# Kernel tuning notes

Measured on AMD Instinct MI355X. Metric: run time of the kernel, lower is better.

The kernel has to match this reference:

```python
import jax, jax.numpy as jnp
import numpy as np

NORMALIZED_LENGTH = 512  # init kwarg
T_FRAMES = 32768
N_LM = 543  # mediapipe holistic landmark count


def setup_inputs() -> dict:
    key = jax.random.key(0)
    kf, kn, kd, ki = jax.random.split(key, 4)
    frames = jax.random.uniform(kf, (T_FRAMES, N_LM, 3), dtype=jnp.float32)
    nan_mask = jax.random.uniform(kn, (T_FRAMES, N_LM, 3)) < 0.10
    frames = jnp.where(nan_mask, jnp.float32(jnp.nan), frames)
    drop = jax.random.uniform(kd, (T_FRAMES,)) < 0.05
    hand_zone = jnp.arange(N_LM) >= 468
    frames = jnp.where(drop[:, None, None] & hand_zone[None, :, None], jnp.float32(jnp.nan), frames)
    lips_idx = jax.random.randint(ki, (40,), 0, 468, dtype=jnp.int32)
    return {"frames": frames, "lips_idx": lips_idx}


def _nan_mean0(x):
    # tf_nan_mean over axis 0 (keepdims); 0/0 -> NaN in TF is immediately zeroed
    # afterwards, so we emit 0 directly (identical forward values, safe grads).
    finite = ~jnp.isnan(x)
    s = jnp.where(finite, x, jnp.zeros((), x.dtype)).sum(axis=0, keepdims=True)
    c = finite.sum(axis=0, keepdims=True)
    return jnp.where(c == 0, jnp.zeros((), x.dtype), s / jnp.maximum(c, 1).astype(x.dtype))


def reference(frames, lips_idx):
    fr = frames[:, :, :2]                       # drop z coord
    lh = fr[:, 468:489]                         # [T, 21, 2]
    rh = fr[:, 522:543]                         # [T, 21, 2]
    lh = jnp.stack([lh[..., 0], 1.0 - lh[..., 1]], axis=-1)
    rh = jnp.stack([1.0 - rh[..., 0], 1.0 - rh[..., 1]], axis=-1)
    # stack hands, NaN->0, sum over the 2-hand axis
    hand = jnp.nan_to_num(lh) + jnp.nan_to_num(rh)   # [T, 21, 2]
    keep = hand.sum(axis=(1, 2)) != 0.0              # frames with >=1 visible hand
    hand = hand[keep]                                # [S, 21, 2]
    lips = fr[:, lips_idx][keep]                     # [S, 40, 2]
    lips = jnp.where(jnp.isnan(lips), _nan_mean0(lips), lips)
    raw = jnp.concatenate([hand, lips], axis=1)      # [S, 61, 2]
    S = int(raw.shape[0])
    # tf.linspace(0, S-1, L+1) cast to int32 -> segment boundaries (truncation)
    b = np.linspace(0.0, S - 1.0, NORMALIZED_LENGTH + 1).astype(np.int32)
    # frame t belongs to bin i with b[i] <= t < b[i+1]; t >= b[L] maps to L (dropped)
    seg = jnp.asarray(np.searchsorted(b, np.arange(S), side="right") - 1)
    sums = jax.ops.segment_sum(raw, seg, num_segments=NORMALIZED_LENGTH)
    cnt = jax.ops.segment_sum(jnp.ones((S,), raw.dtype), seg, num_segments=NORMALIZED_LENGTH)
    # raw is NaN-free at this point, so nan-mean == plain mean; empty bin -> NaN -> 0
    mean = jnp.where(cnt[:, None, None] == 0, jnp.zeros((), raw.dtype),
                     sums / jnp.maximum(cnt, 1.0)[:, None, None])
    sampled = mean.reshape(NORMALIZED_LENGTH, -1)    # Flatten -> [L, 122]
    rows = sampled.sum(axis=1) != 0.0                # drop all-zero (empty) bins
    return sampled[rows]
```

## Files before the change

kernel.cpp:

```cpp
#include <hip/hip_runtime.h>

#define T_FRAMES 32768
#define ROWF 1629
#define NSEG 512
#define NVAL 122
#define PADI 16

__global__ __launch_bounds__(256) void k1_keep(const float* __restrict__ frames,
                                               int* __restrict__ keep) {
  int lane = threadIdx.x & 63;
  int wid = threadIdx.x >> 6;
  int t = blockIdx.x * 4 + wid;
  const float* f = frames + (size_t)t * ROWF;
  float s = 0.0f;
  if (lane < 42) {
    int j = (lane < 21) ? lane : lane - 21;
    int base = ((lane < 21) ? 468 : 522) + j;
    float x = f[base * 3];
    float y = f[base * 3 + 1];
    float ax = (lane < 21) ? x : 1.0f - x;
    float ay = 1.0f - y;
    ax = (ax == ax) ? ax : 0.0f;
    ay = (ay == ay) ? ay : 0.0f;
    s = ax + ay;
  }
  #pragma unroll
  for (int off = 32; off > 0; off >>= 1) s += __shfl_down(s, off);
  if (lane == 0) keep[t] = (s != 0.0f) ? 1 : 0;
}

__global__ __launch_bounds__(1024) void k2_scan(const int* __restrict__ keep,
                                                int* __restrict__ kept_t,
                                                int* __restrict__ Sp) {
  __shared__ int wsum[16];
  int tid = threadIdx.x;
  const int PER = T_FRAMES / 1024;
  int base = tid * PER;
  int fl[PER];
  int local = 0;
  #pragma unroll
  for (int k = 0; k < PER; ++k) { fl[k] = keep[base + k]; local += fl[k]; }

  int lane = tid & 63, wid = tid >> 6;
  int scan = local;
  #pragma unroll
  for (int off = 1; off < 64; off <<= 1) {
    int n = __shfl_up(scan, off);
    if (lane >= off) scan += n;
  }
  if (lane == 63) wsum[wid] = scan;
  __syncthreads();
  if (tid < 16) {
    int v = wsum[tid];
    #pragma unroll
    for (int off = 1; off < 16; off <<= 1) {
      int n = __shfl_up(v, off);
      if (tid >= off) v += n;
    }
    wsum[tid] = v;
  }
  __syncthreads();
  int excl = ((wid == 0) ? 0 : wsum[wid - 1]) + (scan - local);
  #pragma unroll
  for (int k = 0; k < PER; ++k) {
    if (fl[k]) kept_t[excl++] = base + k;
  }
  if (tid == 1023) Sp[0] = wsum[15];
}

__global__ __launch_bounds__(1024) void k3_seg(
    const float* __restrict__ frames, const int* __restrict__ lips_idx,
    const int* __restrict__ kept_t, const int* __restrict__ Sp,
    float* __restrict__ out, int out_size,
    float* __restrict__ seg_ls, int* __restrict__ seg_lc,
    int* __restrict__ seg_n, float* __restrict__ tot_s,
    int* __restrict__ tot_c) {
  __shared__ int seglist[72];
  __shared__ float h_s[42];
  __shared__ float l_s[80];
  __shared__ int   l_c[80];
  int tid = threadIdx.x, lane = tid & 63, wid = tid >> 6;
  int seg = blockIdx.x;
  int S = Sp[0];
  long long M = (long long)S - 1; if (M < 0) M = 0;
  int lo = (int)(((long long)seg * M) >> 9);
  int hi = (int)(((long long)(seg + 1) * M) >> 9);
  int cnt = hi - lo;
  int loadN = cnt + ((seg == NSEG - 1 && S >= 2) ? 1 : 0);

  if (tid < 42) h_s[tid] = 0.0f;
  if (tid < 80) { l_s[tid] = 0.0f; l_c[tid] = 0; }
  if (tid < loadN) seglist[tid] = kept_t[lo + tid];
  __syncthreads();

  int idx1 = 0, idx2 = 0;
  if (lane >= 42) idx1 = lips_idx[lane - 42];
  if (lane < 18)  idx2 = lips_idx[22 + lane];

  float ahx = 0.0f, ahy = 0.0f;
  float a1x = 0.0f, a1y = 0.0f; int c1x = 0, c1y = 0;
  float a2x = 0.0f, a2y = 0.0f; int c2x = 0, c2y = 0;

  for (int k = wid; k < cnt; k += 16) {
    const float* f = frames + (size_t)seglist[k] * ROWF;
    int o1;
    if (lane < 21)      o1 = (468 + lane) * 3;
    else if (lane < 42) o1 = (522 + (lane - 21)) * 3;
    else                o1 = idx1 * 3;
    float x1 = f[o1], y1 = f[o1 + 1];
    float x2 = 0.0f, y2 = 0.0f;
    if (lane < 18) { int o2 = idx2 * 3; x2 = f[o2]; y2 = f[o2 + 1]; }

    float ax = (lane < 21) ? x1 : 1.0f - x1;
    float ay = 1.0f - y1;
    ax = (ax == ax) ? ax : 0.0f;
    ay = (ay == ay) ? ay : 0.0f;
    float bx = __shfl(ax, lane + 21);
    float by = __shfl(ay, lane + 21);
    if (lane < 21) { ahx += ax + bx; ahy += ay + by; }
    if (lane >= 42) {
      if (x1 == x1) { a1x += x1; c1x++; }
      if (y1 == y1) { a1y += y1; c1y++; }
    }
    if (lane < 18) {
      if (x2 == x2) { a2x += x2; c2x++; }
      if (y2 == y2) { a2y += y2; c2y++; }
    }
  }

  if (lane < 21) { atomicAdd(&h_s[2 * lane], ahx); atomicAdd(&h_s[2 * lane + 1], ahy); }
  if (lane >= 42) {
    int j = lane - 42;
    atomicAdd(&l_s[2 * j], a1x); atomicAdd(&l_s[2 * j + 1], a1y);
    atomicAdd(&l_c[2 * j], c1x); atomicAdd(&l_c[2 * j + 1], c1y);
  }
  if (lane < 18) {
    int j = 22 + lane;
    atomicAdd(&l_s[2 * j], a2x); atomicAdd(&l_s[2 * j + 1], a2y);
    atomicAdd(&l_c[2 * j], c2x); atomicAdd(&l_c[2 * j + 1], c2y);
  }
  __syncthreads();

  if (tid < 42) {
    float v = cnt ? h_s[tid] / (float)cnt : 0.0f;
    int o = seg * NVAL + tid;
    if (o < out_size) out[o] = v;
  }
  if (tid < 80) {
    seg_ls[seg * 80 + tid] = l_s[tid];
    seg_lc[seg * 80 + tid] = l_c[tid];
    atomicAdd(&tot_s[tid * PADI], l_s[tid]);
    atomicAdd(&tot_c[tid * PADI], l_c[tid]);
  }
  if (tid == 0) seg_n[seg] = cnt;

  if (seg == NSEG - 1 && S >= 2 && wid == 0 && lane < 40) {
    const float* f = frames + (size_t)seglist[cnt] * ROWF;
    int idx = lips_idx[lane];
    float x = f[idx * 3], y = f[idx * 3 + 1];
    if (x == x) { atomicAdd(&tot_s[(2 * lane) * PADI], x);
                  atomicAdd(&tot_c[(2 * lane) * PADI], 1); }
    if (y == y) { atomicAdd(&tot_s[(2 * lane + 1) * PADI], y);
                  atomicAdd(&tot_c[(2 * lane + 1) * PADI], 1); }
  }
}

__global__ __launch_bounds__(128) void k4_final(
    const float* __restrict__ seg_ls, const int* __restrict__ seg_lc,
    const int* __restrict__ seg_n, const float* __restrict__ tot_s,
    const int* __restrict__ tot_c, float* __restrict__ out, int out_size) {
  int w = threadIdx.x;
  int seg = blockIdx.x;
  if (w >= 80) return;
  int tc = tot_c[w * PADI];
  float cm = tc ? tot_s[w * PADI] / (float)tc : 0.0f;
  int n = seg_n[seg];
  float v = 0.0f;
  if (n) {
    int c = seg_lc[seg * 80 + w];
    v = (seg_ls[seg * 80 + w] + (float)(n - c) * cm) / (float)n;
  }
  int o = seg * NVAL + 42 + w;
  if (o < out_size) out[o] = v;
}

extern "C" void kernel_launch(void* const* d_in, const int* in_sizes, int n_in,
                              void* d_out, int out_size, void* d_ws, size_t ws_size,
                              hipStream_t stream) {
  const float* frames = (const float*)d_in[0];
  const int* lips_idx = (const int*)d_in[1];
  float* out = (float*)d_out;

  char* ws = (char*)d_ws;
  int* keep      = (int*)(ws);
  int* kept_t    = (int*)(ws + 131072);
  int* Sp        = (int*)(ws + 262144);
  float* tot_s   = (float*)(ws + 262208);
  int* tot_c     = (int*)(ws + 267328);
  float* seg_ls  = (float*)(ws + 272448);
  int* seg_lc    = (int*)(ws + 436288);
  int* seg_n     = (int*)(ws + 600128);

  hipMemsetAsync((void*)tot_s, 0, 10240, stream);

  k1_keep<<<8192, 256, 0, stream>>>(frames, keep);
  k2_scan<<<1, 1024, 0, stream>>>(keep, kept_t, Sp);
  k3_seg<<<NSEG, 1024, 0, stream>>>(frames, lips_idx, kept_t, Sp, out, out_size,
                                    seg_ls, seg_lc, seg_n, tot_s, tot_c);
  k4_final<<<NSEG, 128, 0, stream>>>(seg_ls, seg_lc, seg_n, tot_s, tot_c,
                                     out, out_size);
}
```

Before: 300.7 us.

## Fuse keep+scan and seg+final kernels using last-block-done atomic counters

Merges the keep-flag kernel with the single-block scan, and the segment kernel with the finalize kernel. In each case the last block to finish, detected through an atomic counter with threadfences, runs the following stage. This removes two kernel launches and their launch gaps. The trade-off is that the finalize work now runs serially in a single 1024-thread block, and the keep kernel now uses 1024-thread blocks instead of 256.

```diff
diff --git a/kernel.cpp b/kernel.cpp
--- a/kernel.cpp
+++ b/kernel.cpp
@@ -6,16 +6,15 @@
 #define NVAL 122
 #define PADI 16
 
-__global__ __launch_bounds__(256) void k1_keep(const float* __restrict__ frames,
-                                               int* __restrict__ keep) {
-  int lane = threadIdx.x & 63;
-  int wid = threadIdx.x >> 6;
-  int t = blockIdx.x * 4 + wid;
+__global__ __launch_bounds__(1024) void k1_keep_scan(
+    const float* __restrict__ frames, int* __restrict__ keep,
+    int* __restrict__ kept_t, int* __restrict__ Sp, int* __restrict__ ctl) {
+  int tid = threadIdx.x, lane = tid & 63, wid = tid >> 6;
+  int t = blockIdx.x * 16 + wid;
   const float* f = frames + (size_t)t * ROWF;
   float s = 0.0f;
   if (lane < 42) {
-    int j = (lane < 21) ? lane : lane - 21;
-    int base = ((lane < 21) ? 468 : 522) + j;
+    int base = (lane < 21) ? (468 + lane) : (522 + (lane - 21));
     float x = f[base * 3];
     float y = f[base * 3 + 1];
     float ax = (lane < 21) ? x : 1.0f - x;
@@ -27,21 +26,22 @@
   #pragma unroll
   for (int off = 32; off > 0; off >>= 1) s += __shfl_down(s, off);
   if (lane == 0) keep[t] = (s != 0.0f) ? 1 : 0;
-}
-
-__global__ __launch_bounds__(1024) void k2_scan(const int* __restrict__ keep,
-                                                int* __restrict__ kept_t,
-                                                int* __restrict__ Sp) {
+
+  __shared__ int is_last;
+  __threadfence();
+  __syncthreads();
+  if (tid == 0) is_last = (atomicAdd(&ctl[0], 1) == (int)gridDim.x - 1);
+  __syncthreads();
+  if (!is_last) return;
+  __threadfence();
+
   __shared__ int wsum[16];
-  int tid = threadIdx.x;
   const int PER = T_FRAMES / 1024;
   int base = tid * PER;
   int fl[PER];
   int local = 0;
   #pragma unroll
   for (int k = 0; k < PER; ++k) { fl[k] = keep[base + k]; local += fl[k]; }
-
-  int lane = tid & 63, wid = tid >> 6;
   int scan = local;
   #pragma unroll
   for (int off = 1; off < 64; off <<= 1) {
@@ -74,7 +74,7 @@
     float* __restrict__ out, int out_size,
     float* __restrict__ seg_ls, int* __restrict__ seg_lc,
     int* __restrict__ seg_n, float* __restrict__ tot_s,
-    int* __restrict__ tot_c) {
+    int* __restrict__ tot_c, int* __restrict__ ctl) {
   __shared__ int seglist[72];
   __shared__ float h_s[42];
   __shared__ float l_s[80];
@@ -163,25 +163,28 @@
     if (y == y) { atomicAdd(&tot_s[(2 * lane + 1) * PADI], y);
                   atomicAdd(&tot_c[(2 * lane + 1) * PADI], 1); }
   }
-}
-
-__global__ __launch_bounds__(128) void k4_final(
-    const float* __restrict__ seg_ls, const int* __restrict__ seg_lc,
-    const int* __restrict__ seg_n, const float* __restrict__ tot_s,
-    const int* __restrict__ tot_c, float* __restrict__ out, int out_size) {
-  int w = threadIdx.x;
-  int seg = blockIdx.x;
-  if (w >= 80) return;
-  int tc = tot_c[w * PADI];
-  float cm = tc ? tot_s[w * PADI] / (float)tc : 0.0f;
-  int n = seg_n[seg];
-  float v = 0.0f;
-  if (n) {
-    int c = seg_lc[seg * 80 + w];
-    v = (seg_ls[seg * 80 + w] + (float)(n - c) * cm) / (float)n;
-  }
-  int o = seg * NVAL + 42 + w;
-  if (o < out_size) out[o] = v;
+
+  __shared__ int last2;
+  __threadfence();
+  __syncthreads();
+  if (tid == 0) last2 = (atomicAdd(&ctl[16], 1) == NSEG - 1);
+  __syncthreads();
+  if (!last2) return;
+  __threadfence();
+
+  for (int i = tid; i < NSEG * 80; i += 1024) {
+    int sg = i / 80, w = i - sg * 80;
+    int tc = tot_c[w * PADI];
+    float cm = tc ? tot_s[w * PADI] / (float)tc : 0.0f;
+    int n = seg_n[sg];
+    float v = 0.0f;
+    if (n) {
+      int c = seg_lc[sg * 80 + w];
+      v = (seg_ls[sg * 80 + w] + (float)(n - c) * cm) / (float)n;
+    }
+    int o = sg * NVAL + 42 + w;
+    if (o < out_size) out[o] = v;
+  }
 }
 
 extern "C" void kernel_launch(void* const* d_in, const int* in_sizes, int n_in,
@@ -195,18 +198,16 @@
   int* keep      = (int*)(ws);
   int* kept_t    = (int*)(ws + 131072);
   int* Sp        = (int*)(ws + 262144);
-  float* tot_s   = (float*)(ws + 262208);
-  int* tot_c     = (int*)(ws + 267328);
-  float* seg_ls  = (float*)(ws + 272448);
-  int* seg_lc    = (int*)(ws + 436288);
-  int* seg_n     = (int*)(ws + 600128);
-
-  hipMemsetAsync((void*)tot_s, 0, 10240, stream);
-
-  k1_keep<<<8192, 256, 0, stream>>>(frames, keep);
-  k2_scan<<<1, 1024, 0, stream>>>(keep, kept_t, Sp);
+  int* ctl       = (int*)(ws + 262208);
+  float* tot_s   = (float*)(ws + 262336);
+  int* tot_c     = (int*)(ws + 267456);
+  float* seg_ls  = (float*)(ws + 272576);
+  int* seg_lc    = (int*)(ws + 436416);
+  int* seg_n     = (int*)(ws + 600256);
+
+  hipMemsetAsync((void*)ctl, 0, 10368, stream);
+
+  k1_keep_scan<<<2048, 1024, 0, stream>>>(frames, keep, kept_t, Sp, ctl);
   k3_seg<<<NSEG, 1024, 0, stream>>>(frames, lips_idx, kept_t, Sp, out, out_size,
-                                    seg_ls, seg_lc, seg_n, tot_s, tot_c);
-  k4_final<<<NSEG, 128, 0, stream>>>(seg_ls, seg_lc, seg_n, tot_s, tot_c,
-                                     out, out_size);
+                                    seg_ls, seg_lc, seg_n, tot_s, tot_c, ctl);
 }
```

Result: slower. 1.129 ms (+275.4%).

## Replace atomic reductions with per-wave shared partials and single-block final reduce

Applied to the files above, without the earlier changes.

Shared-memory atomics in the segment kernel are replaced by per-wave partial arrays that are summed after the barrier. The global atomic accumulation of lip totals, and the memset that cleared it, are removed. The final kernel becomes one 1024-thread block that reduces the per-segment partials and adds the last kept frame, then writes all outputs. This removes atomic contention and a memset launch, but the final stage now runs on a single block.

```diff
diff --git a/kernel.cpp b/kernel.cpp
--- a/kernel.cpp
+++ b/kernel.cpp
@@ -4,7 +4,7 @@
 #define ROWF 1629
 #define NSEG 512
 #define NVAL 122
-#define PADI 16
+
 
 __global__ __launch_bounds__(256) void k1_keep(const float* __restrict__ frames,
                                                int* __restrict__ keep) {
@@ -14,8 +14,7 @@
   const float* f = frames + (size_t)t * ROWF;
   float s = 0.0f;
   if (lane < 42) {
-    int j = (lane < 21) ? lane : lane - 21;
-    int base = ((lane < 21) ? 468 : 522) + j;
+    int base = (lane < 21) ? (468 + lane) : (522 + (lane - 21));
     float x = f[base * 3];
     float y = f[base * 3 + 1];
     float ax = (lane < 21) ? x : 1.0f - x;
@@ -73,12 +72,11 @@
     const int* __restrict__ kept_t, const int* __restrict__ Sp,
     float* __restrict__ out, int out_size,
     float* __restrict__ seg_ls, int* __restrict__ seg_lc,
-    int* __restrict__ seg_n, float* __restrict__ tot_s,
-    int* __restrict__ tot_c) {
-  __shared__ int seglist[72];
-  __shared__ float h_s[42];
-  __shared__ float l_s[80];
-  __shared__ int   l_c[80];
+    int* __restrict__ seg_n) {
+  __shared__ int seglist[64];
+  __shared__ float hp[16][42];
+  __shared__ float lp[16][80];
+  __shared__ int   cp[16][80];
   int tid = threadIdx.x, lane = tid & 63, wid = tid >> 6;
   int seg = blockIdx.x;
   int S = Sp[0];
@@ -86,11 +84,8 @@
   int lo = (int)(((long long)seg * M) >> 9);
   int hi = (int)(((long long)(seg + 1) * M) >> 9);
   int cnt = hi - lo;
-  int loadN = cnt + ((seg == NSEG - 1 && S >= 2) ? 1 : 0);
-
-  if (tid < 42) h_s[tid] = 0.0f;
-  if (tid < 80) { l_s[tid] = 0.0f; l_c[tid] = 0; }
-  if (tid < loadN) seglist[tid] = kept_t[lo + tid];
+
+  if (tid < cnt) seglist[tid] = kept_t[lo + tid];
   __syncthreads();
 
   int idx1 = 0, idx2 = 0;
@@ -128,60 +123,82 @@
     }
   }
 
-  if (lane < 21) { atomicAdd(&h_s[2 * lane], ahx); atomicAdd(&h_s[2 * lane + 1], ahy); }
+  if (lane < 21) { hp[wid][2 * lane] = ahx; hp[wid][2 * lane + 1] = ahy; }
   if (lane >= 42) {
     int j = lane - 42;
-    atomicAdd(&l_s[2 * j], a1x); atomicAdd(&l_s[2 * j + 1], a1y);
-    atomicAdd(&l_c[2 * j], c1x); atomicAdd(&l_c[2 * j + 1], c1y);
+    lp[wid][2 * j] = a1x; lp[wid][2 * j + 1] = a1y;
+    cp[wid][2 * j] = c1x; cp[wid][2 * j + 1] = c1y;
   }
   if (lane < 18) {
     int j = 22 + lane;
-    atomicAdd(&l_s[2 * j], a2x); atomicAdd(&l_s[2 * j + 1], a2y);
-    atomicAdd(&l_c[2 * j], c2x); atomicAdd(&l_c[2 * j + 1], c2y);
+    lp[wid][2 * j] = a2x; lp[wid][2 * j + 1] = a2y;
+    cp[wid][2 * j] = c2x; cp[wid][2 * j + 1] = c2y;
   }
   __syncthreads();
 
   if (tid < 42) {
-    float v = cnt ? h_s[tid] / (float)cnt : 0.0f;
+    float s = 0.0f;
+    #pragma unroll
+    for (int w = 0; w < 16; ++w) s += hp[w][tid];
+    float v = cnt ? s / (float)cnt : 0.0f;
     int o = seg * NVAL + tid;
     if (o < out_size) out[o] = v;
   }
   if (tid < 80) {
-    seg_ls[seg * 80 + tid] = l_s[tid];
-    seg_lc[seg * 80 + tid] = l_c[tid];
-    atomicAdd(&tot_s[tid * PADI], l_s[tid]);
-    atomicAdd(&tot_c[tid * PADI], l_c[tid]);
+    float s = 0.0f; int c = 0;
+    #pragma unroll
+    for (int w = 0; w < 16; ++w) { s += lp[w][tid]; c += cp[w][tid]; }
+    seg_ls[seg * 80 + tid] = s;
+    seg_lc[seg * 80 + tid] = c;
   }
   if (tid == 0) seg_n[seg] = cnt;
-
-  if (seg == NSEG - 1 && S >= 2 && wid == 0 && lane < 40) {
-    const float* f = frames + (size_t)seglist[cnt] * ROWF;
-    int idx = lips_idx[lane];
-    float x = f[idx * 3], y = f[idx * 3 + 1];
-    if (x == x) { atomicAdd(&tot_s[(2 * lane) * PADI], x);
-                  atomicAdd(&tot_c[(2 * lane) * PADI], 1); }
-    if (y == y) { atomicAdd(&tot_s[(2 * lane + 1) * PADI], y);
-                  atomicAdd(&tot_c[(2 * lane + 1) * PADI], 1); }
-  }
-}
-
-__global__ __launch_bounds__(128) void k4_final(
+}
+
+__global__ __launch_bounds__(1024) void k4_final(
+    const float* __restrict__ frames, const int* __restrict__ lips_idx,
+    const int* __restrict__ kept_t, const int* __restrict__ Sp,
     const float* __restrict__ seg_ls, const int* __restrict__ seg_lc,
-    const int* __restrict__ seg_n, const float* __restrict__ tot_s,
-    const int* __restrict__ tot_c, float* __restrict__ out, int out_size) {
-  int w = threadIdx.x;
-  int seg = blockIdx.x;
-  if (w >= 80) return;
-  int tc = tot_c[w * PADI];
-  float cm = tc ? tot_s[w * PADI] / (float)tc : 0.0f;
-  int n = seg_n[seg];
-  float v = 0.0f;
-  if (n) {
-    int c = seg_lc[seg * 80 + w];
-    v = (seg_ls[seg * 80 + w] + (float)(n - c) * cm) / (float)n;
-  }
-  int o = seg * NVAL + 42 + w;
-  if (o < out_size) out[o] = v;
+    const int* __restrict__ seg_n, float* __restrict__ out, int out_size) {
+  __shared__ float sp[8][80];
+  __shared__ int   scp[8][80];
+  __shared__ float cmv[80];
+  int tid = threadIdx.x;
+  int S = Sp[0];
+
+  if (tid < 640) {
+    int g = tid / 80, w = tid - g * 80;
+    float s = 0.0f; int c = 0;
+    for (int sg = g * 64; sg < g * 64 + 64; ++sg) {
+      s += seg_ls[sg * 80 + w];
+      c += seg_lc[sg * 80 + w];
+    }
+    sp[g][w] = s; scp[g][w] = c;
+  }
+  __syncthreads();
+  if (tid < 80) {
+    float s = 0.0f; int c = 0;
+    #pragma unroll
+    for (int g = 0; g < 8; ++g) { s += sp[g][tid]; c += scp[g][tid]; }
+    if (S >= 1) {
+      int j = tid >> 1, ch = tid & 1;
+      float x = frames[(size_t)kept_t[S - 1] * ROWF + lips_idx[j] * 3 + ch];
+      if (x == x) { s += x; c += 1; }
+    }
+    cmv[tid] = c ? s / (float)c : 0.0f;
+  }
+  __syncthreads();
+
+  for (int i = tid; i < NSEG * 80; i += 1024) {
+    int sg = i / 80, w = i - sg * 80;
+    int n = seg_n[sg];
+    float v = 0.0f;
+    if (n) {
+      int c = seg_lc[sg * 80 + w];
+      v = (seg_ls[sg * 80 + w] + (float)(n - c) * cmv[w]) / (float)n;
+    }
+    int o = sg * NVAL + 42 + w;
+    if (o < out_size) out[o] = v;
+  }
 }
 
 extern "C" void kernel_launch(void* const* d_in, const int* in_sizes, int n_in,
@@ -195,18 +212,14 @@
   int* keep      = (int*)(ws);
   int* kept_t    = (int*)(ws + 131072);
   int* Sp        = (int*)(ws + 262144);
-  float* tot_s   = (float*)(ws + 262208);
-  int* tot_c     = (int*)(ws + 267328);
-  float* seg_ls  = (float*)(ws + 272448);
-  int* seg_lc    = (int*)(ws + 436288);
-  int* seg_n     = (int*)(ws + 600128);
-
-  hipMemsetAsync((void*)tot_s, 0, 10240, stream);
+  float* seg_ls  = (float*)(ws + 262208);
+  int* seg_lc    = (int*)(ws + 426048);
+  int* seg_n     = (int*)(ws + 589888);
 
   k1_keep<<<8192, 256, 0, stream>>>(frames, keep);
   k2_scan<<<1, 1024, 0, stream>>>(keep, kept_t, Sp);
   k3_seg<<<NSEG, 1024, 0, stream>>>(frames, lips_idx, kept_t, Sp, out, out_size,
-                                    seg_ls, seg_lc, seg_n, tot_s, tot_c);
-  k4_final<<<NSEG, 128, 0, stream>>>(seg_ls, seg_lc, seg_n, tot_s, tot_c,
-                                     out, out_size);
-}
+                                    seg_ls, seg_lc, seg_n);
+  k4_final<<<1, 1024, 0, stream>>>(frames, lips_idx, kept_t, Sp,
+                                   seg_ls, seg_lc, seg_n, out, out_size);
+}
```

New measurement: 315.8 us. +5.0%, slower.
